# Kernel optimization log

Hardware: AMD Instinct MI355X
Metric: run time of the kernel (lower is better)

## Reference

```python
import jax, jax.numpy as jnp
import numpy as np

V_NUM = 4
NUM_HEADS = 8


def setup_inputs() -> dict:
    key = jax.random.key(0)
    k1, k2, k3 = jax.random.split(key, 3)
    B, C, H, W = 8, 512, 24, 24
    x = jax.random.normal(k1, (B, C, H, W), dtype=jnp.float32)
    # 1x1 conv weights stored as [out_ch, in_ch]
    w_qkv = jax.random.normal(k2, (3 * C, C), dtype=jnp.float32) * (C ** -0.5)
    w_proj = jax.random.normal(k3, (C, C), dtype=jnp.float32) * (C ** -0.5)
    b_proj = jnp.zeros((C,), dtype=jnp.float32)
    return {"x": x, "w_qkv": w_qkv, "w_proj": w_proj, "b_proj": b_proj}


def reference(x, w_qkv, w_proj, b_proj):
    B, C, H, W = x.shape
    hd = C // NUM_HEADS          # head dim
    scale = hd ** -0.5
    g = B // V_NUM               # batch groups
    N = V_NUM * H * W            # tokens per group

    # 1x1 conv qkv (no bias): [B, 3C, H, W]
    qkv = jnp.einsum('bchw,oc->bohw', x, w_qkv)
    # [g, v, 3C, H, W] -> [g, 3C, v, H, W] -> [g, heads, 3*hd, N]
    t = qkv.reshape(g, V_NUM, 3 * C, H, W).transpose(0, 2, 1, 3, 4)
    t = t.reshape(g, NUM_HEADS, 3 * hd, N)
    q, k, v = jnp.split(t, 3, axis=2)  # each [g, heads, hd, N]

    # attn = k^T @ q * scale : [g, heads, N, N]
    attn = jnp.einsum('ghdn,ghdm->ghnm', k, q) * scale
    attn = jax.nn.softmax(attn, axis=-2)  # softmax over the k axis (dim=-2)

    # out = v @ attn : [g, heads, hd, N]
    out = jnp.einsum('ghdn,ghnm->ghdm', v, attn)
    # [g, C, v, H, W] -> [g, v, C, H, W] -> [B, C, H, W]
    out = out.reshape(g, C, V_NUM, H, W).transpose(0, 2, 1, 3, 4).reshape(B, C, H, W)

    # 1x1 conv proj with bias
    out = jnp.einsum('bchw,oc->bohw', out, w_proj) + b_proj[None, :, None, None]
    return out
```

## Files before the change

### kernel.cpp

```cpp
#include <hip/hip_runtime.h>
#include <stdint.h>

typedef _Float16 f16;
typedef _Float16 half8 __attribute__((ext_vector_type(8)));
typedef _Float16 half4 __attribute__((ext_vector_type(4)));
typedef float floatx4 __attribute__((ext_vector_type(4)));

#define LOG2E 1.44269504088896340736f

__device__ __forceinline__ void async_cp16(const void* g, void* l) {
  __builtin_amdgcn_global_load_lds((const __attribute__((address_space(1))) void*)g,
                                   (__attribute__((address_space(3))) void*)l, 16, 0, 0);
}

__global__ __launch_bounds__(256) void k_transpose_x(const float* __restrict__ x,
                                                     f16* __restrict__ XT) {
  const int hw0 = blockIdx.x * 64, c0 = blockIdx.y * 64, b = blockIdx.z;
  __shared__ f16 sT[64][72];
  const int tid = threadIdx.x;
  const int cc = tid >> 6, hwc = tid & 63;
  const float* xb = x + (size_t)b * 294912;
  for (int i = 0; i < 16; ++i) {
    int c = c0 + i * 4 + cc;
    sT[hwc][i * 4 + cc] = (f16)xb[c * 576 + hw0 + hwc];
  }
  __syncthreads();
  const int c_c = tid & 63, rr = tid >> 6;
  f16* xtb = XT + ((size_t)b * 576 + hw0) * 512 + c0;
  for (int j = 0; j < 16; ++j) {
    int r = j * 4 + rr;
    xtb[(size_t)r * 512 + c_c] = sT[r][c_c];
  }
}

__global__ __launch_bounds__(256) void k_convert_w(const float* __restrict__ wqkv,
                                                   const float* __restrict__ wproj,
                                                   f16* __restrict__ WQ, f16* __restrict__ WP) {
  const float SCALE_Q = 0.125f * LOG2E;
  const int total1 = 1536 * 512, total2 = 512 * 512;
  for (int idx = blockIdx.x * 256 + threadIdx.x; idx < total1 + total2;
       idx += gridDim.x * 256) {
    if (idx < total1) {
      int row = idx >> 9;
      float v = wqkv[idx];
      if ((row % 192) < 64) v *= SCALE_Q;
      WQ[idx] = (f16)v;
    } else {
      WP[idx - total1] = (f16)wproj[idx - total1];
    }
  }
}

__global__ __launch_bounds__(256) void k_qkv_gemm(const f16* __restrict__ XT,
                                                  const f16* __restrict__ WQ,
                                                  f16* __restrict__ Qh, f16* __restrict__ Kh,
                                                  f16* __restrict__ Vt) {
  const int t0 = blockIdx.x * 128, n0 = blockIdx.y * 128;
  __shared__ alignas(16) f16 sA[128 * 64];
  __shared__ alignas(16) f16 sB[128 * 64];
  const int tid = threadIdx.x;
  const int wave = tid >> 6, lane = tid & 63, quad = lane >> 4, l16 = lane & 15;
  const int msub = (wave & 1) * 64, nsub = (wave >> 1) * 64;
  const floatx4 fzero = {0.f, 0.f, 0.f, 0.f};
  floatx4 acc[4][4];
  for (int i = 0; i < 4; ++i)
    for (int j = 0; j < 4; ++j) acc[i][j] = fzero;

  for (int k0 = 0; k0 < 512; k0 += 64) {
    __syncthreads();
    for (int p = 0; p < 4; ++p) {
      int e = p * 256 + tid;
      int row = e >> 3, colb = e & 7;
      async_cp16((const char*)XT + ((size_t)(t0 + row) * 512 + k0 + colb * 8) * 2,
                 (char*)sA + e * 16);
      async_cp16((const char*)WQ + ((size_t)(n0 + row) * 512 + k0 + colb * 8) * 2,
                 (char*)sB + e * 16);
    }
    __syncthreads();
    for (int f = 0; f < 2; ++f) {
      half8 a[4], bfr[4];
      for (int ms = 0; ms < 4; ++ms)
        a[ms] = *(const half8*)&sA[(msub + ms * 16 + l16) * 64 + f * 32 + quad * 8];
      for (int ns = 0; ns < 4; ++ns)
        bfr[ns] = *(const half8*)&sB[(nsub + ns * 16 + l16) * 64 + f * 32 + quad * 8];
      for (int ms = 0; ms < 4; ++ms)
        for (int ns = 0; ns < 4; ++ns)
          acc[ms][ns] =
              __builtin_amdgcn_mfma_f32_16x16x32_f16(a[ms], bfr[ns], acc[ms][ns], 0, 0, 0);
    }
  }
  for (int ms = 0; ms < 4; ++ms) {
    int tbase = t0 + msub + ms * 16 + quad * 4;
    for (int ns = 0; ns < 4; ++ns) {
      int row = n0 + nsub + ns * 16 + l16;
      int h = row / 192, rr2 = row % 192;
      int sel = rr2 >> 6, d = rr2 & 63;
      for (int r = 0; r < 4; ++r) {
        int t = tbase + r;
        int b = t / 576, hw = t % 576;
        int g = b >> 2, v = b & 3;
        int n = v * 576 + hw;
        int gh = g * 8 + h;
        f16 hv = (f16)acc[ms][ns][r];
        size_t idx = ((size_t)gh * 2304 + n) * 64 + d;
        if (sel == 0)
          Qh[idx] = hv;
        else if (sel == 1)
          Kh[idx] = hv;
        else
          Vt[idx] = hv;
      }
    }
  }
}

__global__ __launch_bounds__(256) void k_vtrans(const f16* __restrict__ Vt,
                                                f16* __restrict__ Vh) {
  const int n0 = blockIdx.x * 64, gh = blockIdx.y;
  __shared__ f16 s[64][72];
  const int tid = threadIdx.x;
  {
    int row = tid >> 2, seg = tid & 3;
    const f16* src = Vt + ((size_t)gh * 2304 + n0 + row) * 64 + seg * 16;
    half8 v0 = *(const half8*)src;
    half8 v1 = *(const half8*)(src + 8);
    for (int j = 0; j < 8; ++j) {
      s[row][seg * 16 + j] = v0[j];
      s[row][seg * 16 + 8 + j] = v1[j];
    }
  }
  __syncthreads();
  {
    int d = tid >> 2, nseg = tid & 3;
    f16* dst = Vh + ((size_t)gh * 64 + d) * 2304 + n0 + nseg * 16;
    f16 tmp[16];
    for (int j = 0; j < 16; ++j) tmp[j] = s[nseg * 16 + j][d];
    *(half8*)dst = *(half8*)tmp;
    *(half8*)(dst + 8) = *(half8*)(tmp + 8);
  }
}

__global__ __launch_bounds__(256) void k_attn(const f16* __restrict__ Qh,
                                              const f16* __restrict__ Kh,
                                              const f16* __restrict__ Vh,
                                              f16* __restrict__ AOT) {
  const int mt = blockIdx.x, gh = blockIdx.y;
  const int m0 = mt * 64;
  const int g = gh >> 3, h = gh & 7;
  const f16* Qg = Qh + (size_t)gh * 147456;
  const f16* Kg = Kh + (size_t)gh * 147456;
  const f16* Vg = Vh + (size_t)gh * 147456;
  __shared__ alignas(16) f16 sQ[64 * 64];
  __shared__ alignas(16) f16 sK[2 * 64 * 64];
  __shared__ alignas(16) f16 sV[2 * 64 * 64];
  const int tid = threadIdx.x;
  const int wave = tid >> 6, lane = tid & 63, quad = lane >> 4, l16 = lane & 15;
  const floatx4 fzero = {0.f, 0.f, 0.f, 0.f};
  const int sw = l16 & 7;

  for (int p = 0; p < 2; ++p) {
    int e = p * 256 + tid;
    int row = e >> 3, cb = e & 7, sc = ((cb ^ (row & 7)) << 3);
    async_cp16(Qg + (size_t)(m0 + row) * 64 + sc, (char*)sQ + e * 16);
    async_cp16(Kg + (size_t)row * 64 + sc, (char*)sK + e * 16);
    async_cp16(Vg + (size_t)row * 2304 + sc, (char*)sV + e * 16);
  }
  __syncthreads();

  const int qrow = wave * 16 + l16;
  half8 qa0 = *(const half8*)&sQ[qrow * 64 + ((quad ^ sw) << 3)];
  half8 qa1 = *(const half8*)&sQ[qrow * 64 + (((4 + quad) ^ sw) << 3)];

  for (int p = 0; p < 2; ++p) {
    int e = p * 256 + tid;
    int row = e >> 3, cb = e & 7, sc = ((cb ^ (row & 7)) << 3);
    async_cp16(Kg + (size_t)(64 + row) * 64 + sc, (char*)(sK + 4096) + e * 16);
    async_cp16(Vg + (size_t)row * 2304 + 64 + sc, (char*)(sV + 4096) + e * 16);
  }

  float l_lane = 0.f;
  floatx4 o[4];
  for (int dt = 0; dt < 4; ++dt) o[dt] = fzero;

  for (int kt = 0; kt < 36; ++kt) {
    const f16* bK = sK + (kt & 1) * 4096;
    const f16* bV = sV + (kt & 1) * 4096;

    half4 pf[4];
    for (int nt = 0; nt < 4; ++nt) {
      int krow = nt * 16 + l16;
      half8 kb0 = *(const half8*)&bK[krow * 64 + ((quad ^ sw) << 3)];
      half8 kb1 = *(const half8*)&bK[krow * 64 + (((4 + quad) ^ sw) << 3)];
      floatx4 t = __builtin_amdgcn_mfma_f32_16x16x32_f16(kb0, qa0, fzero, 0, 0, 0);
      t = __builtin_amdgcn_mfma_f32_16x16x32_f16(kb1, qa1, t, 0, 0, 0);
      for (int r = 0; r < 4; ++r) {
        float e = __builtin_amdgcn_exp2f(t[r]);
        l_lane += e;
        pf[nt][r] = (f16)e;
      }
    }
    for (int dt = 0; dt < 4; ++dt) {
      int vrow = dt * 16 + l16;
      for (int nt = 0; nt < 4; ++nt) {
        int chunk = nt * 2 + (quad >> 1);
        half4 vb =
            *(const half4*)&bV[vrow * 64 + ((chunk ^ sw) << 3) + (quad & 1) * 4];
        o[dt] = __builtin_amdgcn_mfma_f32_16x16x16f16(pf[nt], vb, o[dt], 0, 0, 0);
      }
    }

    if (kt < 35) {
      __syncthreads();
      if (kt + 2 < 36) {
        const int n0 = (kt + 2) * 64;
        char* dK = (char*)(sK + (kt & 1) * 4096);
        char* dV = (char*)(sV + (kt & 1) * 4096);
        for (int p = 0; p < 2; ++p) {
          int e = p * 256 + tid;
          int row = e >> 3, cb = e & 7, sc = ((cb ^ (row & 7)) << 3);
          async_cp16(Kg + (size_t)(n0 + row) * 64 + sc, dK + e * 16);
          async_cp16(Vg + (size_t)row * 2304 + n0 + sc, dV + e * 16);
        }
      }
    }
  }

  l_lane += __shfl_xor(l_lane, 16, 64);
  l_lane += __shfl_xor(l_lane, 32, 64);
  float inv[4];
  for (int r = 0; r < 4; ++r) {
    float lr = __shfl(l_lane, quad * 4 + r, 64);
    inv[r] = 1.f / lr;
  }
  for (int dt = 0; dt < 4; ++dt)
    for (int r = 0; r < 4; ++r) {
      int n_tok = m0 + wave * 16 + quad * 4 + r;
      int v = n_tok / 576, hw = n_tok % 576;
      int bb = g * 4 + v;
      int c = h * 64 + dt * 16 + l16;
      AOT[((size_t)bb * 576 + hw) * 512 + c] = (f16)(o[dt][r] * inv[r]);
    }
}

__global__ __launch_bounds__(256) void k_proj_gemm(const f16* __restrict__ AOT,
                                                   const f16* __restrict__ WP,
                                                   const float* __restrict__ bias,
                                                   float* __restrict__ out) {
  const int o0 = blockIdx.x * 128, t0 = blockIdx.y * 128;
  __shared__ alignas(16) f16 sA[128 * 64];
  __shared__ alignas(16) f16 sB[128 * 64];
  const int tid = threadIdx.x;
  const int wave = tid >> 6, lane = tid & 63, quad = lane >> 4, l16 = lane & 15;
  const int msub = (wave & 1) * 64, nsub = (wave >> 1) * 64;
  const floatx4 fzero = {0.f, 0.f, 0.f, 0.f};
  floatx4 acc[4][4];
  for (int i = 0; i < 4; ++i)
    for (int j = 0; j < 4; ++j) acc[i][j] = fzero;

  for (int k0 = 0; k0 < 512; k0 += 64) {
    __syncthreads();
    for (int p = 0; p < 4; ++p) {
      int e = p * 256 + tid;
      int row = e >> 3, colb = e & 7;
      async_cp16((const char*)WP + ((size_t)(o0 + row) * 512 + k0 + colb * 8) * 2,
                 (char*)sA + e * 16);
      async_cp16((const char*)AOT + ((size_t)(t0 + row) * 512 + k0 + colb * 8) * 2,
                 (char*)sB + e * 16);
    }
    __syncthreads();
    for (int f = 0; f < 2; ++f) {
      half8 a[4], bfr[4];
      for (int ms = 0; ms < 4; ++ms)
        a[ms] = *(const half8*)&sA[(msub + ms * 16 + l16) * 64 + f * 32 + quad * 8];
      for (int ns = 0; ns < 4; ++ns)
        bfr[ns] = *(const half8*)&sB[(nsub + ns * 16 + l16) * 64 + f * 32 + quad * 8];
      for (int ms = 0; ms < 4; ++ms)
        for (int ns = 0; ns < 4; ++ns)
          acc[ms][ns] =
              __builtin_amdgcn_mfma_f32_16x16x32_f16(a[ms], bfr[ns], acc[ms][ns], 0, 0, 0);
    }
  }
  for (int ms = 0; ms < 4; ++ms) {
    int o_row = o0 + msub + ms * 16 + quad * 4;
    for (int ns = 0; ns < 4; ++ns) {
      int t = t0 + nsub + ns * 16 + l16;
      int b = t / 576, hw = t % 576;
      for (int r = 0; r < 4; ++r) {
        int orow = o_row + r;
        out[(size_t)b * 294912 + (size_t)orow * 576 + hw] = acc[ms][ns][r] + bias[orow];
      }
    }
  }
}

extern "C" void kernel_launch(void* const* d_in, const int* in_sizes, int n_in,
                              void* d_out, int out_size, void* d_ws, size_t ws_size,
                              hipStream_t stream) {
  const float* x = (const float*)d_in[0];
  const float* wqkv = (const float*)d_in[1];
  const float* wproj = (const float*)d_in[2];
  const float* bias = (const float*)d_in[3];
  float* out = (float*)d_out;
  char* ws = (char*)d_ws;
  f16* XT = (f16*)(ws + 0);
  f16* WQ = (f16*)(ws + 4718592);
  f16* WP = (f16*)(ws + 6291456);
  f16* Qh = (f16*)(ws + 6815744);
  f16* Kh = (f16*)(ws + 11534336);
  f16* Vh = (f16*)(ws + 16252928);
  f16* AOT = (f16*)(ws + 20971520);
  f16* Vt = AOT;

  k_transpose_x<<<dim3(9, 8, 8), dim3(256), 0, stream>>>(x, XT);
  k_convert_w<<<dim3(640), dim3(256), 0, stream>>>(wqkv, wproj, WQ, WP);
  k_qkv_gemm<<<dim3(36, 12), dim3(256), 0, stream>>>(XT, WQ, Qh, Kh, Vt);
  k_vtrans<<<dim3(36, 16), dim3(256), 0, stream>>>(Vt, Vh);
  k_attn<<<dim3(36, 16), dim3(256), 0, stream>>>(Qh, Kh, Vh, AOT);
  k_proj_gemm<<<dim3(4, 36), dim3(256), 0, stream>>>(AOT, WP, bias, out);
}
```

Before: 155.6 us.

## Fuse prep kernels, write V transposed from QKV GEMM, widen attention rows per wave

Merges the x transpose and weight conversion into one launch. The QKV GEMM now writes V directly in d-major layout through an LDS transpose in its epilogue, which removes the separate V transpose kernel and its round trip through global memory. The attention kernel drops to 128 threads, with each wave handling 32 query rows, so every K/V fragment read from LDS feeds twice as many MFMAs. That cuts LDS traffic and launch count at the cost of more registers per thread and fewer waves per block.

Measured after the change: 161.8 us. +4.0%, slower.

```diff
diff --git a/kernel.cpp b/kernel.cpp
--- a/kernel.cpp
+++ b/kernel.cpp
@@ -13,40 +13,41 @@
                                    (__attribute__((address_space(3))) void*)l, 16, 0, 0);
 }
 
-__global__ __launch_bounds__(256) void k_transpose_x(const float* __restrict__ x,
-                                                     f16* __restrict__ XT) {
-  const int hw0 = blockIdx.x * 64, c0 = blockIdx.y * 64, b = blockIdx.z;
+__global__ __launch_bounds__(256) void k_prep(const float* __restrict__ x,
+                                              f16* __restrict__ XT,
+                                              const float* __restrict__ wqkv,
+                                              const float* __restrict__ wproj,
+                                              f16* __restrict__ WQ, f16* __restrict__ WP) {
   __shared__ f16 sT[64][72];
+  const int bid = blockIdx.x;
   const int tid = threadIdx.x;
-  const int cc = tid >> 6, hwc = tid & 63;
-  const float* xb = x + (size_t)b * 294912;
-  for (int i = 0; i < 16; ++i) {
-    int c = c0 + i * 4 + cc;
-    sT[hwc][i * 4 + cc] = (f16)xb[c * 576 + hw0 + hwc];
-  }
-  __syncthreads();
-  const int c_c = tid & 63, rr = tid >> 6;
-  f16* xtb = XT + ((size_t)b * 576 + hw0) * 512 + c0;
-  for (int j = 0; j < 16; ++j) {
-    int r = j * 4 + rr;
-    xtb[(size_t)r * 512 + c_c] = sT[r][c_c];
-  }
-}
-
-__global__ __launch_bounds__(256) void k_convert_w(const float* __restrict__ wqkv,
-                                                   const float* __restrict__ wproj,
-                                                   f16* __restrict__ WQ, f16* __restrict__ WP) {
-  const float SCALE_Q = 0.125f * LOG2E;
-  const int total1 = 1536 * 512, total2 = 512 * 512;
-  for (int idx = blockIdx.x * 256 + threadIdx.x; idx < total1 + total2;
-       idx += gridDim.x * 256) {
-    if (idx < total1) {
-      int row = idx >> 9;
-      float v = wqkv[idx];
-      if ((row % 192) < 64) v *= SCALE_Q;
-      WQ[idx] = (f16)v;
-    } else {
-      WP[idx - total1] = (f16)wproj[idx - total1];
+  if (bid < 576) {
+    const int hw0 = (bid % 9) * 64, c0 = ((bid / 9) & 7) * 64, b = bid / 72;
+    const int cc = tid >> 6, hwc = tid & 63;
+    const float* xb = x + (size_t)b * 294912;
+    for (int i = 0; i < 16; ++i) {
+      int c = c0 + i * 4 + cc;
+      sT[hwc][i * 4 + cc] = (f16)xb[c * 576 + hw0 + hwc];
+    }
+    __syncthreads();
+    const int c_c = tid & 63, rr = tid >> 6;
+    f16* xtb = XT + ((size_t)b * 576 + hw0) * 512 + c0;
+    for (int j = 0; j < 16; ++j) {
+      int r = j * 4 + rr;
+      xtb[(size_t)r * 512 + c_c] = sT[r][c_c];
+    }
+  } else {
+    const float SCALE_Q = 0.125f * LOG2E;
+    const int total1 = 1536 * 512, total2 = 512 * 512;
+    for (int idx = (bid - 576) * 256 + tid; idx < total1 + total2; idx += 128 * 256) {
+      if (idx < total1) {
+        int row = idx >> 9;
+        float v = wqkv[idx];
+        if ((row % 192) < 64) v *= SCALE_Q;
+        WQ[idx] = (f16)v;
+      } else {
+        WP[idx - total1] = (f16)wproj[idx - total1];
+      }
     }
   }
 }
@@ -54,10 +55,11 @@
 __global__ __launch_bounds__(256) void k_qkv_gemm(const f16* __restrict__ XT,
                                                   const f16* __restrict__ WQ,
                                                   f16* __restrict__ Qh, f16* __restrict__ Kh,
-                                                  f16* __restrict__ Vt) {
+                                                  f16* __restrict__ Vh) {
   const int t0 = blockIdx.x * 128, n0 = blockIdx.y * 128;
-  __shared__ alignas(16) f16 sA[128 * 64];
-  __shared__ alignas(16) f16 sB[128 * 64];
+  __shared__ alignas(16) f16 smem[2 * 128 * 64];
+  f16* sA = smem;
+  f16* sB = smem + 128 * 64;
   const int tid = threadIdx.x;
   const int wave = tid >> 6, lane = tid & 63, quad = lane >> 4, l16 = lane & 15;
   const int msub = (wave & 1) * 64, nsub = (wave >> 1) * 64;
@@ -95,6 +97,7 @@
       int row = n0 + nsub + ns * 16 + l16;
       int h = row / 192, rr2 = row % 192;
       int sel = rr2 >> 6, d = rr2 & 63;
+      if (sel == 2) continue;
       for (int r = 0; r < 4; ++r) {
         int t = tbase + r;
         int b = t / 576, hw = t % 576;
@@ -105,42 +108,41 @@
         size_t idx = ((size_t)gh * 2304 + n) * 64 + d;
         if (sel == 0)
           Qh[idx] = hv;
-        else if (sel == 1)
+        else
           Kh[idx] = hv;
-        else
-          Vt[idx] = hv;
-      }
-    }
-  }
-}
-
-__global__ __launch_bounds__(256) void k_vtrans(const f16* __restrict__ Vt,
-                                                f16* __restrict__ Vh) {
-  const int n0 = blockIdx.x * 64, gh = blockIdx.y;
-  __shared__ f16 s[64][72];
-  const int tid = threadIdx.x;
-  {
-    int row = tid >> 2, seg = tid & 3;
-    const f16* src = Vt + ((size_t)gh * 2304 + n0 + row) * 64 + seg * 16;
-    half8 v0 = *(const half8*)src;
-    half8 v1 = *(const half8*)(src + 8);
-    for (int j = 0; j < 8; ++j) {
-      s[row][seg * 16 + j] = v0[j];
-      s[row][seg * 16 + 8 + j] = v1[j];
-    }
-  }
-  __syncthreads();
-  {
-    int d = tid >> 2, nseg = tid & 3;
-    f16* dst = Vh + ((size_t)gh * 64 + d) * 2304 + n0 + nseg * 16;
-    f16 tmp[16];
-    for (int j = 0; j < 16; ++j) tmp[j] = s[nseg * 16 + j][d];
-    *(half8*)dst = *(half8*)tmp;
-    *(half8*)(dst + 8) = *(half8*)(tmp + 8);
-  }
-}
-
-__global__ __launch_bounds__(256) void k_attn(const f16* __restrict__ Qh,
+      }
+    }
+  }
+  const int r0 = n0 % 192;
+  if (r0 != 0) {
+    const int vloc = (r0 == 128) ? 0 : 64;
+    const int h = (n0 + vloc) / 192;
+    f16* sVT = smem;
+    __syncthreads();
+    if ((wave >> 1) == (vloc >> 6)) {
+      for (int ms = 0; ms < 4; ++ms) {
+        int tok = msub + ms * 16 + quad * 4;
+        for (int ns = 0; ns < 4; ++ns) {
+          int d = ns * 16 + l16;
+          half4 hv;
+          for (int r = 0; r < 4; ++r) hv[r] = (f16)acc[ms][ns][r];
+          *(half4*)&sVT[d * 136 + tok] = hv;
+        }
+      }
+    }
+    __syncthreads();
+    for (int pss = 0; pss < 4; ++pss) {
+      int d = pss * 16 + (tid >> 4), chunk = tid & 15;
+      int t = t0 + chunk * 8;
+      int b = t / 576, hw = t - b * 576;
+      int gh = (b >> 2) * 8 + h, n = (b & 3) * 576 + hw;
+      *(half8*)(Vh + (size_t)gh * 147456 + (size_t)d * 2304 + n) =
+          *(const half8*)&sVT[d * 136 + chunk * 8];
+    }
+  }
+}
+
+__global__ __launch_bounds__(128) void k_attn(const f16* __restrict__ Qh,
                                               const f16* __restrict__ Kh,
                                               const f16* __restrict__ Vh,
                                               f16* __restrict__ AOT) {
@@ -158,8 +160,8 @@
   const floatx4 fzero = {0.f, 0.f, 0.f, 0.f};
   const int sw = l16 & 7;
 
-  for (int p = 0; p < 2; ++p) {
-    int e = p * 256 + tid;
+  for (int p = 0; p < 4; ++p) {
+    int e = p * 128 + tid;
     int row = e >> 3, cb = e & 7, sc = ((cb ^ (row & 7)) << 3);
     async_cp16(Qg + (size_t)(m0 + row) * 64 + sc, (char*)sQ + e * 16);
     async_cp16(Kg + (size_t)row * 64 + sc, (char*)sK + e * 16);
@@ -167,45 +169,51 @@
   }
   __syncthreads();
 
-  const int qrow = wave * 16 + l16;
-  half8 qa0 = *(const half8*)&sQ[qrow * 64 + ((quad ^ sw) << 3)];
-  half8 qa1 = *(const half8*)&sQ[qrow * 64 + (((4 + quad) ^ sw) << 3)];
-
-  for (int p = 0; p < 2; ++p) {
-    int e = p * 256 + tid;
+  half8 qa[2][2];
+  for (int s = 0; s < 2; ++s) {
+    int qrow = wave * 32 + s * 16 + l16;
+    qa[s][0] = *(const half8*)&sQ[qrow * 64 + ((quad ^ sw) << 3)];
+    qa[s][1] = *(const half8*)&sQ[qrow * 64 + (((4 + quad) ^ sw) << 3)];
+  }
+
+  for (int p = 0; p < 4; ++p) {
+    int e = p * 128 + tid;
     int row = e >> 3, cb = e & 7, sc = ((cb ^ (row & 7)) << 3);
     async_cp16(Kg + (size_t)(64 + row) * 64 + sc, (char*)(sK + 4096) + e * 16);
     async_cp16(Vg + (size_t)row * 2304 + 64 + sc, (char*)(sV + 4096) + e * 16);
   }
 
-  float l_lane = 0.f;
-  floatx4 o[4];
-  for (int dt = 0; dt < 4; ++dt) o[dt] = fzero;
+  float l_lane[2] = {0.f, 0.f};
+  floatx4 o[2][4];
+  for (int s = 0; s < 2; ++s)
+    for (int dt = 0; dt < 4; ++dt) o[s][dt] = fzero;
 
   for (int kt = 0; kt < 36; ++kt) {
     const f16* bK = sK + (kt & 1) * 4096;
     const f16* bV = sV + (kt & 1) * 4096;
 
-    half4 pf[4];
+    half4 pf[2][4];
     for (int nt = 0; nt < 4; ++nt) {
       int krow = nt * 16 + l16;
       half8 kb0 = *(const half8*)&bK[krow * 64 + ((quad ^ sw) << 3)];
       half8 kb1 = *(const half8*)&bK[krow * 64 + (((4 + quad) ^ sw) << 3)];
-      floatx4 t = __builtin_amdgcn_mfma_f32_16x16x32_f16(kb0, qa0, fzero, 0, 0, 0);
-      t = __builtin_amdgcn_mfma_f32_16x16x32_f16(kb1, qa1, t, 0, 0, 0);
-      for (int r = 0; r < 4; ++r) {
-        float e = __builtin_amdgcn_exp2f(t[r]);
-        l_lane += e;
-        pf[nt][r] = (f16)e;
+      for (int s = 0; s < 2; ++s) {
+        floatx4 t = __builtin_amdgcn_mfma_f32_16x16x32_f16(kb0, qa[s][0], fzero, 0, 0, 0);
+        t = __builtin_amdgcn_mfma_f32_16x16x32_f16(kb1, qa[s][1], t, 0, 0, 0);
+        for (int r = 0; r < 4; ++r) {
+          float e = __builtin_amdgcn_exp2f(t[r]);
+          l_lane[s] += e;
+          pf[s][nt][r] = (f16)e;
+        }
       }
     }
     for (int dt = 0; dt < 4; ++dt) {
       int vrow = dt * 16 + l16;
       for (int nt = 0; nt < 4; ++nt) {
         int chunk = nt * 2 + (quad >> 1);
-        half4 vb =
-            *(const half4*)&bV[vrow * 64 + ((chunk ^ sw) << 3) + (quad & 1) * 4];
-        o[dt] = __builtin_amdgcn_mfma_f32_16x16x16f16(pf[nt], vb, o[dt], 0, 0, 0);
+        half4 vb = *(const half4*)&bV[vrow * 64 + ((chunk ^ sw) << 3) + (quad & 1) * 4];
+        for (int s = 0; s < 2; ++s)
+          o[s][dt] = __builtin_amdgcn_mfma_f32_16x16x16f16(pf[s][nt], vb, o[s][dt], 0, 0, 0);
       }
     }
 
@@ -215,8 +223,8 @@
         const int n0 = (kt + 2) * 64;
         char* dK = (char*)(sK + (kt & 1) * 4096);
         char* dV = (char*)(sV + (kt & 1) * 4096);
-        for (int p = 0; p < 2; ++p) {
-          int e = p * 256 + tid;
+        for (int p = 0; p < 4; ++p) {
+          int e = p * 128 + tid;
           int row = e >> 3, cb = e & 7, sc = ((cb ^ (row & 7)) << 3);
           async_cp16(Kg + (size_t)(n0 + row) * 64 + sc, dK + e * 16);
           async_cp16(Vg + (size_t)row * 2304 + n0 + sc, dV + e * 16);
@@ -225,21 +233,25 @@
     }
   }
 
-  l_lane += __shfl_xor(l_lane, 16, 64);
-  l_lane += __shfl_xor(l_lane, 32, 64);
-  float inv[4];
-  for (int r = 0; r < 4; ++r) {
-    float lr = __shfl(l_lane, quad * 4 + r, 64);
-    inv[r] = 1.f / lr;
-  }
-  for (int dt = 0; dt < 4; ++dt)
+  for (int s = 0; s < 2; ++s) {
+    l_lane[s] += __shfl_xor(l_lane[s], 16, 64);
+    l_lane[s] += __shfl_xor(l_lane[s], 32, 64);
+  }
+  for (int s = 0; s < 2; ++s) {
+    float inv[4];
     for (int r = 0; r < 4; ++r) {
-      int n_tok = m0 + wave * 16 + quad * 4 + r;
-      int v = n_tok / 576, hw = n_tok % 576;
-      int bb = g * 4 + v;
-      int c = h * 64 + dt * 16 + l16;
-      AOT[((size_t)bb * 576 + hw) * 512 + c] = (f16)(o[dt][r] * inv[r]);
-    }
+      float lr = __shfl(l_lane[s], quad * 4 + r, 64);
+      inv[r] = 1.f / lr;
+    }
+    for (int dt = 0; dt < 4; ++dt)
+      for (int r = 0; r < 4; ++r) {
+        int n_tok = m0 + wave * 32 + s * 16 + quad * 4 + r;
+        int v = n_tok / 576, hw = n_tok % 576;
+        int bb = g * 4 + v;
+        int c = h * 64 + dt * 16 + l16;
+        AOT[((size_t)bb * 576 + hw) * 512 + c] = (f16)(o[s][dt][r] * inv[r]);
+      }
+  }
 }
 
 __global__ __launch_bounds__(256) void k_proj_gemm(const f16* __restrict__ AOT,
@@ -309,12 +321,9 @@
   f16* Kh = (f16*)(ws + 11534336);
   f16* Vh = (f16*)(ws + 16252928);
   f16* AOT = (f16*)(ws + 20971520);
-  f16* Vt = AOT;
-
-  k_transpose_x<<<dim3(9, 8, 8), dim3(256), 0, stream>>>(x, XT);
-  k_convert_w<<<dim3(640), dim3(256), 0, stream>>>(wqkv, wproj, WQ, WP);
-  k_qkv_gemm<<<dim3(36, 12), dim3(256), 0, stream>>>(XT, WQ, Qh, Kh, Vt);
-  k_vtrans<<<dim3(36, 16), dim3(256), 0, stream>>>(Vt, Vh);
-  k_attn<<<dim3(36, 16), dim3(256), 0, stream>>>(Qh, Kh, Vh, AOT);
+
+  k_prep<<<dim3(704), dim3(256), 0, stream>>>(x, XT, wqkv, wproj, WQ, WP);
+  k_qkv_gemm<<<dim3(36, 12), dim3(256), 0, stream>>>(XT, WQ, Qh, Kh, Vh);
+  k_attn<<<dim3(36, 16), dim3(128), 0, stream>>>(Qh, Kh, Vh, AOT);
   k_proj_gemm<<<dim3(4, 36), dim3(256), 0, stream>>>(AOT, WP, bias, out);
 }
```
